# Optimization experiments

Measured on AMD Instinct MI355X. Metric: run time of the kernel, lower is better.

The kernel has to match this reference:

```python
import jax, jax.numpy as jnp
import numpy as np

N = 50000
K = 4
D_IN = 256
D_OUT = 64
E = 800000

def setup_inputs() -> dict:
    key = jax.random.key(0)
    k1, k2, k3, k4, k5 = jax.random.split(key, 5)
    x = jax.random.normal(k1, (N, K, D_IN), dtype=jnp.float32)
    weight = jax.random.normal(k2, (D_IN, D_OUT), dtype=jnp.float32) * (1.0 / np.sqrt(D_IN))
    adj_rows = jax.random.randint(k3, (E,), 0, N, dtype=jnp.int32)
    adj_cols = jax.random.randint(k4, (E,), 0, N, dtype=jnp.int32)
    adj_vals = jax.random.uniform(k5, (E,), dtype=jnp.float32)
    return {"x": x, "weight": weight, "adj_rows": adj_rows, "adj_cols": adj_cols, "adj_vals": adj_vals}

def reference(x, weight, adj_rows, adj_cols, adj_vals):
    # x: [N, K, D_in]; weight: [D_in, D_out]
    # dropout p=0.0 / eval mode -> identity
    # support = x @ W for every sample k, vectorized over K
    support = jnp.einsum('nkd,df->nkf', x, weight)          # [N, K, D_out]
    # sparse adj matmul: out[r] += vals[e] * support[cols[e]]
    msgs = adj_vals[:, None, None] * support[adj_cols]       # [E, K, D_out]
    out = jax.ops.segment_sum(msgs, adj_rows, num_segments=N)  # [N, K, D_out]
    return jax.nn.relu(out)
```

## Files before the change

### kernel.cpp

```cpp
#include <hip/hip_runtime.h>
#include <stdint.h>

#define D_IN   256
#define D_OUT  64
#define KHEADS 4
#define ROWLEN 256
#define GBM    128
#define LDW    264
#define WBT_B  (64 * LDW * 2)
#define CAP    128
#define EPB    512

typedef __attribute__((ext_vector_type(8))) short bf16x8;
typedef __attribute__((ext_vector_type(4))) float f32x4;

__device__ __forceinline__ unsigned cvt_pk_bf16(float lo, float hi) {
  unsigned r;
  asm("v_cvt_pk_bf16_f32 %0, %1, %2" : "=v"(r) : "v"(lo), "v"(hi));
  return r;
}

__device__ __forceinline__ bf16x8 pack8(float4 a, float4 b) {
  union { unsigned u[4]; bf16x8 v; } r;
  r.u[0] = cvt_pk_bf16(a.x, a.y);
  r.u[1] = cvt_pk_bf16(a.z, a.w);
  r.u[2] = cvt_pk_bf16(b.x, b.y);
  r.u[3] = cvt_pk_bf16(b.z, b.w);
  return r.v;
}

__global__ __launch_bounds__(256) void prep_w(const float* __restrict__ W,
                                              unsigned short* __restrict__ WbT) {
  int idx = blockIdx.x * 256 + threadIdx.x;
  int n  = idx >> 6;
  int k0 = (idx & 63) << 2;
  float w0 = W[(size_t)(k0 + 0) * D_OUT + n];
  float w1 = W[(size_t)(k0 + 1) * D_OUT + n];
  float w2 = W[(size_t)(k0 + 2) * D_OUT + n];
  float w3 = W[(size_t)(k0 + 3) * D_OUT + n];
  unsigned p0 = cvt_pk_bf16(w0, w1);
  unsigned p1 = cvt_pk_bf16(w2, w3);
  *(uint2*)&WbT[(size_t)n * LDW + k0] = make_uint2(p0, p1);
}

__global__ __launch_bounds__(256) void fused_gemm_place(
    const float* __restrict__ X, const unsigned short* __restrict__ WbT,
    signed char* __restrict__ SqH, float* __restrict__ scaleArr,
    const int* __restrict__ rows, const int* __restrict__ cols,
    const float* __restrict__ vals, int* __restrict__ cnt,
    uint2* __restrict__ ecv, int M, int Nnodes, int E) {
  __shared__ __align__(16) unsigned short lWt[64 * LDW];
  const int t    = threadIdx.x;
  const int g    = blockIdx.x;

  {
    int base = g * EPB + t;
#pragma unroll
    for (int u = 0; u < 2; ++u) {
      int e = base + u * 256;
      if (e < E) {
        int r = rows[e];
        int c = cols[e];
        float v = vals[e];
        int pos = atomicAdd(&cnt[r], 1);
        if (pos < CAP)
          ecv[((size_t)r << 7) + pos] = make_uint2((unsigned)c, __float_as_uint(v));
      }
    }
  }

  {
    const uint4* __restrict__ src = (const uint4*)WbT;
    uint4* dst = (uint4*)lWt;
#pragma unroll
    for (int r2 = 0; r2 < 9; ++r2) {
      int slot = t + r2 * 256;
      if (slot < WBT_B / 16) dst[slot] = src[slot];
    }
  }
  __syncthreads();

  const int wave = t >> 6;
  const int lane = t & 63;
  const int q    = lane >> 4;
  const int l16  = lane & 15;
  const long row0 = (long)g * GBM;

  long r0 = row0 + wave * 32 + l16;       if (r0 > (long)M - 1) r0 = M - 1;
  long r1 = row0 + wave * 32 + 16 + l16;  if (r1 > (long)M - 1) r1 = M - 1;
  const float* __restrict__ x0 = X + r0 * D_IN + q * 8;
  const float* __restrict__ x1 = X + r1 * D_IN + q * 8;

  f32x4 acc[2][4];
#pragma unroll
  for (int rb = 0; rb < 2; ++rb)
#pragma unroll
    for (int cb = 0; cb < 4; ++cb) acc[rb][cb] = (f32x4){0.f, 0.f, 0.f, 0.f};

  float4 c00 = *(const float4*)(x0);
  float4 c01 = *(const float4*)(x0 + 4);
  float4 c10 = *(const float4*)(x1);
  float4 c11 = *(const float4*)(x1 + 4);
#pragma unroll
  for (int s = 0; s < 8; ++s) {
    float4 n00, n01, n10, n11;
    if (s < 7) {
      const float* p0 = x0 + (s + 1) * 32;
      const float* p1 = x1 + (s + 1) * 32;
      n00 = *(const float4*)(p0); n01 = *(const float4*)(p0 + 4);
      n10 = *(const float4*)(p1); n11 = *(const float4*)(p1 + 4);
    }
    bf16x8 a0 = pack8(c00, c01);
    bf16x8 a1 = pack8(c10, c11);
    const unsigned short* wb = &lWt[l16 * LDW + s * 32 + q * 8];
#pragma unroll
    for (int cb = 0; cb < 4; ++cb) {
      bf16x8 b = *(const bf16x8*)(wb + cb * 16 * LDW);
      acc[0][cb] = __builtin_amdgcn_mfma_f32_16x16x32_bf16(a0, b, acc[0][cb], 0, 0, 0);
      acc[1][cb] = __builtin_amdgcn_mfma_f32_16x16x32_bf16(a1, b, acc[1][cb], 0, 0, 0);
    }
    if (s < 7) { c00 = n00; c01 = n01; c10 = n10; c11 = n11; }
  }

  float nm0 = 0.f, nm1 = 0.f;
#pragma unroll
  for (int cb = 0; cb < 4; ++cb)
#pragma unroll
    for (int reg = 0; reg < 4; ++reg) {
      nm0 = fmaxf(nm0, fabsf(acc[0][cb][reg]));
      nm1 = fmaxf(nm1, fabsf(acc[1][cb][reg]));
    }
#pragma unroll
  for (int d = 1; d < 16; d <<= 1) {
    nm0 = fmaxf(nm0, __shfl_xor(nm0, d, 64));
    nm1 = fmaxf(nm1, __shfl_xor(nm1, d, 64));
  }
  const float inv0 = (nm0 > 0.f) ? 127.f / nm0 : 0.f;
  const float inv1 = (nm1 > 0.f) ? 127.f / nm1 : 0.f;
  const int node_base = g * 32 + wave * 8;
  if (l16 == 0) {
    int n0 = node_base + q;
    int n1 = node_base + 4 + q;
    if (n0 < Nnodes) scaleArr[n0] = nm0 / 127.f;
    if (n1 < Nnodes) scaleArr[n1] = nm1 / 127.f;
  }
#pragma unroll
  for (int rb = 0; rb < 2; ++rb) {
    const float inv = rb ? inv1 : inv0;
#pragma unroll
    for (int cb = 0; cb < 4; ++cb)
#pragma unroll
      for (int reg = 0; reg < 4; ++reg) {
        long r = row0 + wave * 32 + rb * 16 + q * 4 + reg;
        if (r < M) {
          int qi = (int)rintf(acc[rb][cb][reg] * inv);
          int node = (int)(r >> 2);
          int head = (int)(r & 3);
          SqH[((size_t)head * Nnodes + node) * 64 + cb * 16 + l16] = (signed char)qi;
        }
      }
  }
}

__global__ __launch_bounds__(256) void gather_kernel(
    const signed char* __restrict__ SqH, const float* __restrict__ scaleArr,
    const int* __restrict__ cnt, const uint2* __restrict__ ecv,
    float* __restrict__ out, int n, int bph) {
  const int bid  = blockIdx.x;
  const int head = bid / bph;
  const int rb   = (bid - head * bph) * 4 + (threadIdx.x >> 6);
  if (rb >= n) return;
  const int lane = threadIdx.x & 63;
  const int e2   = lane >> 4;
  const int d16  = lane & 15;
  int deg = cnt[rb];
  if (deg > CAP) deg = CAP;
  const uint2* __restrict__ bucket = ecv + ((size_t)rb << 7);

  unsigned long long bl = *((const unsigned long long*)bucket + lane);
  const unsigned mc = (lane < deg) ? (unsigned)bl : 0u;
  const float    mv = (lane < deg)
      ? __uint_as_float((unsigned)(bl >> 32)) * scaleArr[mc] : 0.f;

  const int* __restrict__ Sh = (const int*)SqH + (size_t)head * (size_t)n * 16;

  float4 aA = make_float4(0.f, 0.f, 0.f, 0.f);
  float4 aB = aA;
  const int d0  = deg < 64 ? deg : 64;
  const int nd0 = (d0 + 7) & ~7;
  for (int i = 0; i < nd0; i += 8) {
    const int eA = i + e2;
    const int eB = i + 4 + e2;
    const unsigned cA = __shfl(mc, eA);
    const unsigned cB = __shfl(mc, eB);
    const float    vA = __shfl(mv, eA);
    const float    vB = __shfl(mv, eB);
    const int wA = Sh[(size_t)cA * 16 + d16];
    const int wB = Sh[(size_t)cB * 16 + d16];
    aA.x += vA * (float)(wA << 24 >> 24); aA.y += vA * (float)(wA << 16 >> 24);
    aA.z += vA * (float)(wA <<  8 >> 24); aA.w += vA * (float)(wA >> 24);
    aB.x += vB * (float)(wB << 24 >> 24); aB.y += vB * (float)(wB << 16 >> 24);
    aB.z += vB * (float)(wB <<  8 >> 24); aB.w += vB * (float)(wB >> 24);
  }
  if (deg > 64) {
    unsigned long long bl1 = *((const unsigned long long*)bucket + 64 + lane);
    const unsigned mc1 = (64 + lane < deg) ? (unsigned)bl1 : 0u;
    const float    mv1 = (64 + lane < deg)
        ? __uint_as_float((unsigned)(bl1 >> 32)) * scaleArr[mc1] : 0.f;
    const int ndt = (deg + 3) & ~3;
    for (int i = 64; i < ndt; i += 4) {
      const int idx = i + e2 - 64;
      const unsigned cA = __shfl(mc1, idx);
      const float    vA = __shfl(mv1, idx);
      const int wA = Sh[(size_t)cA * 16 + d16];
      aA.x += vA * (float)(wA << 24 >> 24); aA.y += vA * (float)(wA << 16 >> 24);
      aA.z += vA * (float)(wA <<  8 >> 24); aA.w += vA * (float)(wA >> 24);
    }
  }
  float4 a;
  a.x = aA.x + aB.x; a.y = aA.y + aB.y; a.z = aA.z + aB.z; a.w = aA.w + aB.w;
  a.x += __shfl_xor(a.x, 16, 64); a.y += __shfl_xor(a.y, 16, 64);
  a.z += __shfl_xor(a.z, 16, 64); a.w += __shfl_xor(a.w, 16, 64);
  a.x += __shfl_xor(a.x, 32, 64); a.y += __shfl_xor(a.y, 32, 64);
  a.z += __shfl_xor(a.z, 32, 64); a.w += __shfl_xor(a.w, 32, 64);
  if (e2 == 0) {
    f32x4 res;
    res[0] = fmaxf(a.x, 0.f);
    res[1] = fmaxf(a.y, 0.f);
    res[2] = fmaxf(a.z, 0.f);
    res[3] = fmaxf(a.w, 0.f);
    __builtin_nontemporal_store(
        res, (f32x4*)&out[(size_t)rb * ROWLEN + head * 64 + (d16 << 2)]);
  }
}

extern "C" void kernel_launch(void* const* d_in, const int* in_sizes, int n_in,
                              void* d_out, int out_size, void* d_ws, size_t ws_size,
                              hipStream_t stream) {
  const float* x    = (const float*)d_in[0];
  const float* w    = (const float*)d_in[1];
  const int*   rows = (const int*)d_in[2];
  const int*   cols = (const int*)d_in[3];
  const float* vals = (const float*)d_in[4];
  float* out = (float*)d_out;

  const int E = in_sizes[2];
  const int N = in_sizes[0] / (KHEADS * D_IN);
  const int M = N * KHEADS;

  char* ws = (char*)d_ws;
  size_t o = 0;
  signed char* SqH = (signed char*)(ws + o); o += (size_t)M * D_OUT;
  o = (o + 15) & ~(size_t)15;
  float* scaleArr = (float*)(ws + o); o += (size_t)N * sizeof(float);
  o = (o + 15) & ~(size_t)15;
  int* cnt = (int*)(ws + o); o += (size_t)N * sizeof(int);
  o = (o + 63) & ~(size_t)63;
  unsigned short* WbT = (unsigned short*)(ws + o); o += WBT_B;
  o = (o + 15) & ~(size_t)15;
  uint2* ecv = (uint2*)(ws + o);

  hipMemsetAsync(cnt, 0, (size_t)N * sizeof(int), stream);

  int G = (M + GBM - 1) / GBM;
  const int Ge = (E + EPB - 1) / EPB;
  if (Ge > G) G = Ge;
  prep_w<<<16, 256, 0, stream>>>(w, WbT);
  fused_gemm_place<<<G, 256, 0, stream>>>(x, WbT, SqH, scaleArr, rows, cols,
                                          vals, cnt, ecv, M, N, E);
  const int bph = (N + 3) / 4;
  gather_kernel<<<bph * KHEADS, 256, 0, stream>>>(SqH, scaleArr, cnt, ecv,
                                                  out, N, bph);
}
```

Before: 419.3 us.

## Split edge placement from GEMM and deepen X prefetch pipeline

Moves the edge bucketing (atomic counts and ecv writes) out of the fused GEMM kernel into its own launch, so the GEMM kernel no longer waits on scattered atomics. The GEMM kernel now issues its first two X-tile loads before staging W into LDS and keeps a three-slot register ring, prefetching two steps ahead. It also adds a min-blocks-per-CU launch bound. The cost is an extra kernel launch and a separate pass over the edge arrays, with no overlap between placement and the GEMM, plus higher register pressure from the deeper prefetch.

```diff
diff --git a/kernel.cpp b/kernel.cpp
--- a/kernel.cpp
+++ b/kernel.cpp
@@ -9,7 +9,6 @@
 #define LDW    264
 #define WBT_B  (64 * LDW * 2)
 #define CAP    128
-#define EPB    512
 
 typedef __attribute__((ext_vector_type(8))) short bf16x8;
 typedef __attribute__((ext_vector_type(4))) float f32x4;
@@ -43,43 +42,29 @@
   *(uint2*)&WbT[(size_t)n * LDW + k0] = make_uint2(p0, p1);
 }
 
-__global__ __launch_bounds__(256) void fused_gemm_place(
+__global__ __launch_bounds__(256) void place_kernel(const int* __restrict__ rows,
+                                                    const int* __restrict__ cols,
+                                                    const float* __restrict__ vals,
+                                                    int* __restrict__ cnt,
+                                                    uint2* __restrict__ ecv, int E) {
+  int e = blockIdx.x * 256 + threadIdx.x;
+  if (e < E) {
+    int r = rows[e];
+    int c = cols[e];
+    float v = vals[e];
+    int pos = atomicAdd(&cnt[r], 1);
+    if (pos < CAP)
+      ecv[((size_t)r << 7) + pos] = make_uint2((unsigned)c, __float_as_uint(v));
+  }
+}
+
+__global__ __launch_bounds__(256, 4) void gemm_kernel(
     const float* __restrict__ X, const unsigned short* __restrict__ WbT,
     signed char* __restrict__ SqH, float* __restrict__ scaleArr,
-    const int* __restrict__ rows, const int* __restrict__ cols,
-    const float* __restrict__ vals, int* __restrict__ cnt,
-    uint2* __restrict__ ecv, int M, int Nnodes, int E) {
+    int M, int Nnodes) {
   __shared__ __align__(16) unsigned short lWt[64 * LDW];
   const int t    = threadIdx.x;
   const int g    = blockIdx.x;
-
-  {
-    int base = g * EPB + t;
-#pragma unroll
-    for (int u = 0; u < 2; ++u) {
-      int e = base + u * 256;
-      if (e < E) {
-        int r = rows[e];
-        int c = cols[e];
-        float v = vals[e];
-        int pos = atomicAdd(&cnt[r], 1);
-        if (pos < CAP)
-          ecv[((size_t)r << 7) + pos] = make_uint2((unsigned)c, __float_as_uint(v));
-      }
-    }
-  }
-
-  {
-    const uint4* __restrict__ src = (const uint4*)WbT;
-    uint4* dst = (uint4*)lWt;
-#pragma unroll
-    for (int r2 = 0; r2 < 9; ++r2) {
-      int slot = t + r2 * 256;
-      if (slot < WBT_B / 16) dst[slot] = src[slot];
-    }
-  }
-  __syncthreads();
-
   const int wave = t >> 6;
   const int lane = t & 63;
   const int q    = lane >> 4;
@@ -91,27 +76,44 @@
   const float* __restrict__ x0 = X + r0 * D_IN + q * 8;
   const float* __restrict__ x1 = X + r1 * D_IN + q * 8;
 
+  float4 p[3][4];
+#pragma unroll
+  for (int s = 0; s < 2; ++s) {
+    p[s][0] = *(const float4*)(x0 + s * 32);
+    p[s][1] = *(const float4*)(x0 + s * 32 + 4);
+    p[s][2] = *(const float4*)(x1 + s * 32);
+    p[s][3] = *(const float4*)(x1 + s * 32 + 4);
+  }
+
+  {
+    const uint4* __restrict__ src = (const uint4*)WbT;
+    uint4* dst = (uint4*)lWt;
+#pragma unroll
+    for (int r2 = 0; r2 < 9; ++r2) {
+      int slot = t + r2 * 256;
+      if (slot < WBT_B / 16) dst[slot] = src[slot];
+    }
+  }
+  __syncthreads();
+
   f32x4 acc[2][4];
 #pragma unroll
   for (int rb = 0; rb < 2; ++rb)
 #pragma unroll
     for (int cb = 0; cb < 4; ++cb) acc[rb][cb] = (f32x4){0.f, 0.f, 0.f, 0.f};
 
-  float4 c00 = *(const float4*)(x0);
-  float4 c01 = *(const float4*)(x0 + 4);
-  float4 c10 = *(const float4*)(x1);
-  float4 c11 = *(const float4*)(x1 + 4);
 #pragma unroll
   for (int s = 0; s < 8; ++s) {
-    float4 n00, n01, n10, n11;
-    if (s < 7) {
-      const float* p0 = x0 + (s + 1) * 32;
-      const float* p1 = x1 + (s + 1) * 32;
-      n00 = *(const float4*)(p0); n01 = *(const float4*)(p0 + 4);
-      n10 = *(const float4*)(p1); n11 = *(const float4*)(p1 + 4);
-    }
-    bf16x8 a0 = pack8(c00, c01);
-    bf16x8 a1 = pack8(c10, c11);
+    const int cs = s % 3;
+    if (s + 2 < 8) {
+      const int ns = (s + 2) % 3;
+      p[ns][0] = *(const float4*)(x0 + (s + 2) * 32);
+      p[ns][1] = *(const float4*)(x0 + (s + 2) * 32 + 4);
+      p[ns][2] = *(const float4*)(x1 + (s + 2) * 32);
+      p[ns][3] = *(const float4*)(x1 + (s + 2) * 32 + 4);
+    }
+    bf16x8 a0 = pack8(p[cs][0], p[cs][1]);
+    bf16x8 a1 = pack8(p[cs][2], p[cs][3]);
     const unsigned short* wb = &lWt[l16 * LDW + s * 32 + q * 8];
 #pragma unroll
     for (int cb = 0; cb < 4; ++cb) {
@@ -119,7 +121,6 @@
       acc[0][cb] = __builtin_amdgcn_mfma_f32_16x16x32_bf16(a0, b, acc[0][cb], 0, 0, 0);
       acc[1][cb] = __builtin_amdgcn_mfma_f32_16x16x32_bf16(a1, b, acc[1][cb], 0, 0, 0);
     }
-    if (s < 7) { c00 = n00; c01 = n01; c10 = n10; c11 = n11; }
   }
 
   float nm0 = 0.f, nm1 = 0.f;
@@ -262,12 +263,11 @@
 
   hipMemsetAsync(cnt, 0, (size_t)N * sizeof(int), stream);
 
-  int G = (M + GBM - 1) / GBM;
-  const int Ge = (E + EPB - 1) / EPB;
-  if (Ge > G) G = Ge;
+  const int G = (M + GBM - 1) / GBM;
+  const int P = (E + 255) / 256;
   prep_w<<<16, 256, 0, stream>>>(w, WbT);
-  fused_gemm_place<<<G, 256, 0, stream>>>(x, WbT, SqH, scaleArr, rows, cols,
-                                          vals, cnt, ecv, M, N, E);
+  place_kernel<<<P, 256, 0, stream>>>(rows, cols, vals, cnt, ecv, E);
+  gemm_kernel<<<G, 256, 0, stream>>>(x, WbT, SqH, scaleArr, M, N);
   const int bph = (N + 3) / 4;
   gather_kernel<<<bph * KHEADS, 256, 0, stream>>>(SqH, scaleArr, cnt, ecv,
                                                   out, N, bph);
```

New measurement: 431.2 us. +2.8%, slower.
